# Kernel optimization log

Measured on AMD Instinct MI355X. Metric: run time of the kernel, lower is better.

## Reference

```python
import jax, jax.numpy as jnp
import numpy as np

E = 64  # hidden size (hardcoded in the module)
D = 50  # embedding dim (hardcoded)


def lstm_scan(xs, h0, c0, Wih, Whh, b):
    """xs: (S, B, in). PyTorch gate order i, f, g, o."""
    def step(carry, x):
        h, c = carry
        g = x @ Wih.T + h @ Whh.T + b
        i, f, gg, o = jnp.split(g, 4, axis=-1)
        c = jax.nn.sigmoid(f) * c + jax.nn.sigmoid(i) * jnp.tanh(gg)
        h = jax.nn.sigmoid(o) * jnp.tanh(c)
        return (h, c), (h, c)
    _, (hs, cs) = jax.lax.scan(step, (h0, c0), xs)
    return hs, cs  # (S, B, E)


def setup_inputs() -> dict:
    key = jax.random.key(0)
    ks = iter(jax.random.split(key, 40))
    B, S, V = 64, 384, 100004
    f32 = jnp.float32

    def rn(shape, scale):
        return (jax.random.normal(next(ks), shape, dtype=f32) * scale)

    km = float(np.sqrt(2.0 / E))       # kaiming_normal fan_in=64
    lu = float(1.0 / np.sqrt(E))       # torch LSTM default init scale

    inp = {
        "sentence1": jax.random.randint(next(ks), (B, S), 0, V),
        "sentence2": jax.random.randint(next(ks), (B, S), 0, V),
        "s1_len": jax.random.randint(next(ks), (B, 1, E), 0, S),
        "s2_len": jax.random.randint(next(ks), (B, 1, E), 0, S),
        "s1_s": jnp.ones((B, S), dtype=f32),
        "s2_s": jnp.ones((B, S), dtype=f32),
        "emb": rn((V, D), 0.1),
        "Wih1": rn((4 * E, D), lu), "Whh1": rn((4 * E, E), lu),
        "bih1": rn((4 * E,), lu), "bhh1": rn((4 * E,), lu),
        "Wih2": rn((4 * E, D), lu), "Whh2": rn((4 * E, E), lu),
        "bih2": rn((4 * E,), lu), "bhh2": rn((4 * E,), lu),
        "wy": rn((E, E), km), "wh": rn((E, E), km),
        "w": rn((E,), 1.0),
        "wp": rn((E, E), km), "wx": rn((E, E), km),
        "wr": rn((E, E), km), "wt": rn((E, E), km),
        "l1_W": rn((128, E), km), "l1_b": jnp.zeros((128,), f32),
        "l_W": rn((4, 128), float(np.sqrt(2.0 / 128))), "l_b": jnp.zeros((4,), f32),
    }
    return inp


def reference(sentence1, sentence2, s1_len, s2_len, s1_s, s2_s, emb,
              Wih1, Whh1, bih1, bhh1, Wih2, Whh2, bih2, bhh2,
              wy, wh, w, wp, wx, wr, wt, l1_W, l1_b, l_W, l_b):
    B, S = sentence1.shape
    e1 = emb[sentence1]  # (B,S,50)
    e2 = emb[sentence2]
    h0 = jnp.zeros((B, E), e1.dtype)

    # LSTMCell loop over sentence1, collecting all h/c
    hs, cs = lstm_scan(e1.transpose(1, 0, 2), h0, h0, Wih1, Whh1, bih1 + bhh1)
    h = hs.transpose(1, 0, 2)  # (B,S,E)
    c = cs.transpose(1, 0, 2)

    # gather initial state for lstm2 at s1_len indices
    gh = jnp.take_along_axis(h, s1_len, axis=1)[:, 0, :]
    gc = jnp.take_along_axis(c, s1_len, axis=1)[:, 0, :]

    os_, _ = lstm_scan(e2.transpose(1, 0, 2), gh, gc, Wih2, Whh2, bih2 + bhh2)
    out = os_.transpose(1, 0, 2)  # (B,S,E); note s2 == s per expand semantics

    # wyy + whhn are loop-invariant in the original (out.expand is identity)
    base = jnp.einsum('bse,ef->bsf', h, wy) + jnp.einsum('bse,ef->bsf', out, wh)
    NEG = jnp.float32(1e12)

    def att_step(r, _):
        M = jnp.tanh(base + (r @ wr)[:, None, :])          # (B,S,E)
        score = jnp.einsum('bse,e->bs', M, w)              # (B,S)
        masked = s1_s * score - (1.0 - s1_s) * NEG
        soft = jax.nn.softmax(masked, axis=1)
        r_new = jnp.einsum('bse,bs->be', h, soft) + jnp.tanh(r @ wt)
        return r_new, r_new

    r0 = jnp.zeros((B, E), h.dtype)
    _, Rt = jax.lax.scan(att_step, r0, None, length=S)
    Rt = Rt.transpose(1, 0, 2)  # (B,S,E)

    rn_ = jnp.take_along_axis(Rt, s2_len, axis=1)[:, 0, :]
    hn = jnp.take_along_axis(out, s2_len, axis=1)[:, 0, :]
    hid = jnp.tanh(rn_ @ wp + hn @ wx)
    hid = jnp.tanh(hid @ l1_W.T + l1_b)   # Dropout is inference-mode identity
    return hid @ l_W.T + l_b              # (B,4)
```

## Files before the change

### kernel.cpp

```cpp
#include <hip/hip_runtime.h>

#define E 64
#define D 50
#define SS 384
#define G4 256

__device__ __forceinline__ float fast_rcp(float x){ return __builtin_amdgcn_rcpf(x); }
__device__ __forceinline__ float tanh_fast(float x){
  float e = __expf(2.0f*x);
  return 1.0f - 2.0f*fast_rcp(e + 1.0f);
}
__device__ __forceinline__ float sigmoid_fast(float x){
  return fast_rcp(1.0f + __expf(-x));
}
__device__ __forceinline__ float rdlane(float v, int l){
  return __int_as_float(__builtin_amdgcn_readlane(__float_as_int(v), l));
}
#define DPP0(x, ctrl) __int_as_float(__builtin_amdgcn_update_dpp( \
    0, __float_as_int(x), ctrl, 0xF, 0xF, true))
__device__ __forceinline__ float wave_sum64_l63(float x){
  x += DPP0(x, 0x111);
  x += DPP0(x, 0x112);
  x += DPP0(x, 0x114);
  x += DPP0(x, 0x118);
  x += DPP0(x, 0x142);
  x += DPP0(x, 0x143);
  return x;
}
__device__ __forceinline__ void barrier_lds_only(){
  __builtin_amdgcn_sched_barrier(0);
  asm volatile("s_waitcnt lgkmcnt(0)" ::: "memory");
  __builtin_amdgcn_s_barrier();
  __builtin_amdgcn_sched_barrier(0);
}

__global__ __launch_bounds__(256, 1) void gx_kernel(
  const int* __restrict__ sent1, const int* __restrict__ sent2,
  const float* __restrict__ emb,
  const float* __restrict__ Wih1, const float* __restrict__ bih1, const float* __restrict__ bhh1,
  const float* __restrict__ Wih2, const float* __restrict__ bih2, const float* __restrict__ bhh2,
  float* __restrict__ gx1, float* __restrict__ gx2)
{
  const int bb    = blockIdx.x;
  const int which = bb >> 8;
  const int chunk = bb & 255;
  const int j     = threadIdx.x;
  const int*   sent = which ? sent2 : sent1;
  const float* Wih  = which ? Wih2  : Wih1;
  const float* bA   = which ? bih2  : bih1;
  const float* bB   = which ? bhh2  : bhh1;
  float*       gx   = which ? gx2   : gx1;

  float wih[D];
  #pragma unroll
  for (int k=0;k<D;k+=2){
    float2 v = *(const float2*)&Wih[j*D+k];
    wih[k]=v.x; wih[k+1]=v.y;
  }
  const float bias = bA[j] + bB[j];

  __shared__ __align__(16) float xb[8][52];
  const int row0 = chunk*96;
  for (int c=0;c<12;++c){
    const int r0 = row0 + c*8;
    #pragma unroll
    for (int q=0;q<2;++q){
      int tt = j + q*256;
      if (tt < 400){
        int r = tt/50;
        int k = tt - r*50;
        int idx = sent[r0 + r];
        xb[r][k] = emb[(size_t)idx*D + k];
      }
    }
    __syncthreads();
    for (int r=0;r<8;++r){
      float a0=bias, a1=0.f;
      #pragma unroll
      for (int k=0;k<48;k+=4){
        float4 xv = *(const float4*)&xb[r][k];
        a0 += xv.x*wih[k]   + xv.y*wih[k+1];
        a1 += xv.z*wih[k+2] + xv.w*wih[k+3];
      }
      a0 += xb[r][48]*wih[48];
      a1 += xb[r][49]*wih[49];
      gx[(size_t)(r0+r)*G4 + j] = a0+a1;
    }
    __syncthreads();
  }
}

__global__ __launch_bounds__(256, 1) void lstm_kernel(
  const float* __restrict__ gx1, const float* __restrict__ gx2,
  const float* __restrict__ Whh1, const float* __restrict__ Whh2,
  const int* __restrict__ s1_len, const int* __restrict__ s2_len,
  float* __restrict__ h1_all, float* __restrict__ out_all,
  float* __restrict__ hn_cap)
{
  const int b = blockIdx.x;
  const int j = threadIdx.x;
  const int lane = j & 63;
  const int wv = j >> 6;
  __shared__ float gates[2][256];
  __shared__ __align__(16) float hbuf[4][64];

  float whr[64];
  #pragma unroll
  for (int k=0;k<64;k+=4){
    float4 v = *(const float4*)&Whh1[j*64+k];
    whr[k]=v.x; whr[k+1]=v.y; whr[k+2]=v.z; whr[k+3]=v.w;
  }

  const int is_g = (wv==2);
  float c_reg=0.f, h_reg=0.f, gh=0.f, gc=0.f, hn=0.f;
  const int idx1 = s1_len[b*64+lane];
  const int idx2 = s2_len[b*64+lane];
  hbuf[wv][lane] = 0.f;

  {
    const float* gx = gx1 + (size_t)b*SS*G4;
    float* hout = h1_all + (size_t)b*SS*E;
    float gx_cur = gx[j];
    float gx_n1  = gx[G4 + j];
    float h_prev = 0.f;
    for (int s=0;s<SS;++s){
      int sn2 = (s+2<SS)? s+2 : SS-1;
      float gx_n2 = gx[(size_t)sn2*G4 + j];
      float g0=gx_cur, g1=0.f, g2=0.f, g3=0.f;
      #pragma unroll
      for (int k=0;k<64;k+=4){
        float4 hv = *(const float4*)&hbuf[wv][k];
        g0 = __builtin_fmaf(hv.x, whr[k],   g0);
        g1 = __builtin_fmaf(hv.y, whr[k+1], g1);
        g2 = __builtin_fmaf(hv.z, whr[k+2], g2);
        g3 = __builtin_fmaf(hv.w, whr[k+3], g3);
      }
      float g = (g0+g1)+(g2+g3);
      const int p = s & 1;
      gates[p][j] = is_g ? tanh_fast(g) : sigmoid_fast(g);
      barrier_lds_only();
      float gi=gates[p][lane], gf=gates[p][64+lane], gg=gates[p][128+lane], go=gates[p][192+lane];
      c_reg = gf*c_reg + gi*gg;
      h_reg = go * tanh_fast(c_reg);
      hbuf[wv][lane] = h_reg;
      if (wv==0 && s>0) hout[(size_t)(s-1)*E + lane] = h_prev;
      h_prev = h_reg;
      if (s==idx1){ gh=h_reg; gc=c_reg; }
      gx_cur = gx_n1; gx_n1 = gx_n2;
    }
    if (wv==0) hout[(size_t)(SS-1)*E + lane] = h_prev;
  }
  #pragma unroll
  for (int k=0;k<64;k+=4){
    float4 v = *(const float4*)&Whh2[j*64+k];
    whr[k]=v.x; whr[k+1]=v.y; whr[k+2]=v.z; whr[k+3]=v.w;
  }
  h_reg = gh; c_reg = gc;
  hbuf[wv][lane] = gh;
  barrier_lds_only();
  {
    const float* gx = gx2 + (size_t)b*SS*G4;
    float* hout = out_all + (size_t)b*SS*E;
    float gx_cur = gx[j];
    float gx_n1  = gx[G4 + j];
    float h_prev = 0.f;
    for (int s=0;s<SS;++s){
      int sn2 = (s+2<SS)? s+2 : SS-1;
      float gx_n2 = gx[(size_t)sn2*G4 + j];
      float g0=gx_cur, g1=0.f, g2=0.f, g3=0.f;
      #pragma unroll
      for (int k=0;k<64;k+=4){
        float4 hv = *(const float4*)&hbuf[wv][k];
        g0 = __builtin_fmaf(hv.x, whr[k],   g0);
        g1 = __builtin_fmaf(hv.y, whr[k+1], g1);
        g2 = __builtin_fmaf(hv.z, whr[k+2], g2);
        g3 = __builtin_fmaf(hv.w, whr[k+3], g3);
      }
      float g = (g0+g1)+(g2+g3);
      const int p = s & 1;
      gates[p][j] = is_g ? tanh_fast(g) : sigmoid_fast(g);
      barrier_lds_only();
      float gi=gates[p][lane], gf=gates[p][64+lane], gg=gates[p][128+lane], go=gates[p][192+lane];
      c_reg = gf*c_reg + gi*gg;
      h_reg = go * tanh_fast(c_reg);
      hbuf[wv][lane] = h_reg;
      if (wv==0 && s>0) hout[(size_t)(s-1)*E + lane] = h_prev;
      h_prev = h_reg;
      if (s==idx2) hn = h_reg;
      gx_cur = gx_n1; gx_n1 = gx_n2;
    }
    if (wv==0) hout[(size_t)(SS-1)*E + lane] = h_prev;
  }
  if (wv==0) hn_cap[b*64+lane] = hn;
}

__global__ __launch_bounds__(256, 1) void base_kernel(
  const float* __restrict__ h1_all, const float* __restrict__ out_all,
  const float* __restrict__ wy, const float* __restrict__ wh,
  float* __restrict__ E_g)
{
  const int t = threadIdx.x;
  const int wave = t>>6, lane = t&63;
  float wyc[E], whc[E];
  #pragma unroll
  for (int e=0;e<E;++e){ wyc[e]=wy[e*E+lane]; whc[e]=wh[e*E+lane]; }
  const int row0 = blockIdx.x*16 + wave*4;
  for (int r=0;r<4;++r){
    int row = row0 + r;
    float hv = h1_all[(size_t)row*E + lane];
    float ov = out_all[(size_t)row*E + lane];
    float a0=0,a1=0;
    #pragma unroll
    for (int e=0;e<E;++e){
      a0 += rdlane(hv,e)*wyc[e];
      a1 += rdlane(ov,e)*whc[e];
    }
    E_g[(size_t)row*E + lane] = __expf(2.0f*(a0+a1));
  }
}

__global__ __attribute__((amdgpu_flat_work_group_size(384,384), amdgpu_waves_per_eu(2,2)))
void attn_kernel(
  const float* __restrict__ h1_all, const float* __restrict__ E_all,
  const float* __restrict__ w, const float* __restrict__ wr, const float* __restrict__ wt,
  const float* __restrict__ s1_s, const int* __restrict__ s2_len,
  float* __restrict__ rn_cap)
{
  const int b = blockIdx.x;
  const int t = threadIdx.x;
  const int wv = t>>6, lane = t&63;
  const int row = wv*64 + lane;

  __shared__ float  accP[6*64];
  __shared__ float  totP[8];
  __shared__ float2 rwrtP[6*64];
  __shared__ __align__(16) float exL[6][64];
  __shared__ __align__(16) float RlL[6][64];

  const float* h1b = h1_all + (size_t)b*SS*E;
  const float* Eb  = E_all  + (size_t)b*SS*E;

  float Ee[64];
  #pragma unroll
  for (int k=0;k<64;k+=4){
    float4 v = *(const float4*)&Eb[(size_t)row*E + k];
    Ee[k]=v.x; Ee[k+1]=v.y; Ee[k+2]=v.z; Ee[k+3]=v.w;
  }
  float ht[64];
  #pragma unroll
  for (int i=0;i<64;++i){
    ht[i] = h1b[(size_t)(wv*64 + i)*E + lane];
  }
  float WSUM = 0.f;
  for (int e=0;e<64;++e) WSUM += w[e];
  const float s1v = s1_s[b*SS + row];
  const int  idx2 = s2_len[b*E + lane];
  const int k0  = (wv<4)? wv*11 : 44+(wv-4)*10;
  const int cnt = (wv<4)? 11 : 10;
  float wrch[11], wtch[11];
  #pragma unroll
  for (int jj=0;jj<11;++jj){
    int kk = k0 + ((jj<cnt)? jj : 0);
    wrch[jj] = wr[kk*E + lane];
    wtch[jj] = wt[kk*E + lane];
  }

  rwrtP[t] = make_float2(0.f, 0.f);
  __syncthreads();

  float rn_keep = 0.f;
  for (int s=0;s<SS;++s){
    float rwl=0.f, rtl=0.f;
    #pragma unroll
    for (int q=0;q<6;++q){ float2 v = rwrtP[q*64+lane]; rwl+=v.x; rtl+=v.y; }
    float Rl = __expf(2.0f*rwl);
    RlL[wv][lane] = Rl;

    float sc0=0.f, sc1=0.f, sc2=0.f, sc3=0.f;
    #pragma unroll
    for (int e=0;e<64;e+=8){
      float4 ra = *(const float4*)&RlL[wv][e];
      float4 rb = *(const float4*)&RlL[wv][e+4];
      float A  = __builtin_fmaf(Ee[e],  ra.x, 1.f);
      float B  = __builtin_fmaf(Ee[e+1],ra.y, 1.f);
      float C  = __builtin_fmaf(Ee[e+2],ra.z, 1.f);
      float Dv = __builtin_fmaf(Ee[e+3],ra.w, 1.f);
      float n0 = __builtin_fmaf(w[e],   B,  w[e+1]*A);
      float n1 = __builtin_fmaf(w[e+2], Dv, w[e+3]*C);
      sc0 = __builtin_fmaf(n0, fast_rcp(A*B),  sc0);
      sc1 = __builtin_fmaf(n1, fast_rcp(C*Dv), sc1);
      float A2  = __builtin_fmaf(Ee[e+4], rb.x, 1.f);
      float B2  = __builtin_fmaf(Ee[e+5], rb.y, 1.f);
      float C2  = __builtin_fmaf(Ee[e+6], rb.z, 1.f);
      float D2  = __builtin_fmaf(Ee[e+7], rb.w, 1.f);
      float n2 = __builtin_fmaf(w[e+4], B2, w[e+5]*A2);
      float n3 = __builtin_fmaf(w[e+6], D2, w[e+7]*C2);
      sc2 = __builtin_fmaf(n2, fast_rcp(A2*B2), sc2);
      sc3 = __builtin_fmaf(n3, fast_rcp(C2*D2), sc3);
    }
    float sc = WSUM - 2.0f*((sc0+sc1)+(sc2+sc3));
    float masked = s1v*sc - (1.f - s1v)*1e12f;
    float ex = __expf(masked);

    exL[wv][lane] = ex;
    float a0=0.f, a1=0.f, a2=0.f, a3=0.f;
    #pragma unroll
    for (int i=0;i<64;i+=4){
      float4 v = *(const float4*)&exL[wv][i];
      a0 = __builtin_fmaf(v.x, ht[i],   a0);
      a1 = __builtin_fmaf(v.y, ht[i+1], a1);
      a2 = __builtin_fmaf(v.z, ht[i+2], a2);
      a3 = __builtin_fmaf(v.w, ht[i+3], a3);
    }
    accP[wv*64+lane] = (a0+a1)+(a2+a3);
    float tw = wave_sum64_l63(ex);
    if (lane==63) totP[wv] = tw;
    __syncthreads();

    float av=0.f;
    #pragma unroll
    for (int q=0;q<6;++q) av += accP[q*64+lane];
    float tv = ((totP[0]+totP[1])+(totP[2]+totP[3]))+(totP[4]+totP[5]);
    float rnew = __builtin_fmaf(av, fast_rcp(tv), tanh_fast(rtl));
    if (wv==0 && s==idx2) rn_keep = rnew;
    float rwp=0.f, rtp=0.f;
    #pragma unroll
    for (int jj=0;jj<11;++jj){
      if (jj<cnt){
        float rv = rdlane(rnew, k0+jj);
        rwp = __builtin_fmaf(rv, wrch[jj], rwp);
        rtp = __builtin_fmaf(rv, wtch[jj], rtp);
      }
    }
    rwrtP[wv*64+lane] = make_float2(rwp, rtp);
    __syncthreads();
  }
  if (wv==0) rn_cap[b*E + lane] = rn_keep;
}

__global__ __launch_bounds__(128, 1) void final_kernel(
  const float* __restrict__ rn_cap, const float* __restrict__ hn_cap,
  const float* __restrict__ wp, const float* __restrict__ wx,
  const float* __restrict__ l1W, const float* __restrict__ l1b,
  const float* __restrict__ lW, const float* __restrict__ lb,
  float* __restrict__ out)
{
  const int b = blockIdx.x, t = threadIdx.x;
  __shared__ float rn[E], hn[E], hid1[E], hid2[128];
  if (t<E){ rn[t]=rn_cap[b*E+t]; hn[t]=hn_cap[b*E+t]; }
  __syncthreads();
  if (t<E){
    float a0=0,a1=0;
    #pragma unroll
    for (int k=0;k<E;++k){
      a0 += rn[k]*wp[k*E+t];
      a1 += hn[k]*wx[k*E+t];
    }
    hid1[t] = tanh_fast(a0+a1);
  }
  __syncthreads();
  {
    float acc = l1b[t];
    #pragma unroll
    for (int k=0;k<E;++k) acc += hid1[k]*l1W[t*E+k];
    hid2[t] = tanh_fast(acc);
  }
  __syncthreads();
  if (t<4){
    float acc = lb[t];
    #pragma unroll
    for (int k=0;k<128;++k) acc += hid2[k]*lW[t*128+k];
    out[b*4+t] = acc;
  }
}

extern "C" void kernel_launch(void* const* d_in, const int* in_sizes, int n_in,
                              void* d_out, int out_size, void* d_ws, size_t ws_size,
                              hipStream_t stream)
{
  const int*   sent1 = (const int*)  d_in[0];
  const int*   sent2 = (const int*)  d_in[1];
  const int*   s1len = (const int*)  d_in[2];
  const int*   s2len = (const int*)  d_in[3];
  const float* s1s   = (const float*)d_in[4];
  const float* emb   = (const float*)d_in[6];
  const float* Wih1  = (const float*)d_in[7];
  const float* Whh1  = (const float*)d_in[8];
  const float* bih1  = (const float*)d_in[9];
  const float* bhh1  = (const float*)d_in[10];
  const float* Wih2  = (const float*)d_in[11];
  const float* Whh2  = (const float*)d_in[12];
  const float* bih2  = (const float*)d_in[13];
  const float* bhh2  = (const float*)d_in[14];
  const float* wy    = (const float*)d_in[15];
  const float* wh    = (const float*)d_in[16];
  const float* w     = (const float*)d_in[17];
  const float* wp    = (const float*)d_in[18];
  const float* wx    = (const float*)d_in[19];
  const float* wr    = (const float*)d_in[20];
  const float* wt    = (const float*)d_in[21];
  const float* l1W   = (const float*)d_in[22];
  const float* l1b   = (const float*)d_in[23];
  const float* lW    = (const float*)d_in[24];
  const float* lb    = (const float*)d_in[25];
  float* out = (float*)d_out;

  float* ws  = (float*)d_ws;
  float* gx1 = ws;
  float* gx2 = gx1 + 6291456;
  float* h1  = gx2 + 6291456;
  float* outa= h1  + 1572864;
  float* Eg  = outa + 1572864;
  float* rnc = Eg  + 1572864;
  float* hnc = rnc + 4096;

  hipLaunchKernelGGL(gx_kernel, dim3(512), dim3(256), 0, stream,
    sent1, sent2, emb, Wih1, bih1, bhh1, Wih2, bih2, bhh2, gx1, gx2);
  hipLaunchKernelGGL(lstm_kernel, dim3(64), dim3(256), 0, stream,
    gx1, gx2, Whh1, Whh2, s1len, s2len, h1, outa, hnc);
  hipLaunchKernelGGL(base_kernel, dim3(1536), dim3(256), 0, stream,
    h1, outa, wy, wh, Eg);
  hipLaunchKernelGGL(attn_kernel, dim3(64), dim3(384), 0, stream,
    h1, Eg, w, wr, wt, s1s, s2len, rnc);
  hipLaunchKernelGGL(final_kernel, dim3(64), dim3(128), 0, stream,
    rnc, hnc, wp, wx, l1W, l1b, lW, lb, out);
}
```

Baseline: 1.329 ms.

## Pack two batch elements per workgroup in LSTM and attention kernels

```diff
diff --git a/kernel.cpp b/kernel.cpp
--- a/kernel.cpp
+++ b/kernel.cpp
@@ -90,46 +90,49 @@
   }
 }
 
-__global__ __launch_bounds__(256, 1) void lstm_kernel(
+__global__ __launch_bounds__(512, 1) void lstm_kernel(
   const float* __restrict__ gx1, const float* __restrict__ gx2,
   const float* __restrict__ Whh1, const float* __restrict__ Whh2,
   const int* __restrict__ s1_len, const int* __restrict__ s2_len,
   float* __restrict__ h1_all, float* __restrict__ out_all,
   float* __restrict__ hn_cap)
 {
-  const int b = blockIdx.x;
-  const int j = threadIdx.x;
-  const int lane = j & 63;
-  const int wv = j >> 6;
-  __shared__ float gates[2][256];
-  __shared__ __align__(16) float hbuf[4][64];
+  const int j    = threadIdx.x;
+  const int grp  = j >> 8;
+  const int jL   = j & 255;
+  const int b    = blockIdx.x*2 + grp;
+  const int lane = jL & 63;
+  const int wvL  = jL >> 6;
+  const int gw   = j >> 6;
+  __shared__ float gates[2][2][256];
+  __shared__ __align__(16) float hbuf[8][64];
 
   float whr[64];
   #pragma unroll
   for (int k=0;k<64;k+=4){
-    float4 v = *(const float4*)&Whh1[j*64+k];
+    float4 v = *(const float4*)&Whh1[jL*64+k];
     whr[k]=v.x; whr[k+1]=v.y; whr[k+2]=v.z; whr[k+3]=v.w;
   }
 
-  const int is_g = (wv==2);
+  const int is_g = (wvL==2);
   float c_reg=0.f, h_reg=0.f, gh=0.f, gc=0.f, hn=0.f;
   const int idx1 = s1_len[b*64+lane];
   const int idx2 = s2_len[b*64+lane];
-  hbuf[wv][lane] = 0.f;
+  hbuf[gw][lane] = 0.f;
 
   {
     const float* gx = gx1 + (size_t)b*SS*G4;
     float* hout = h1_all + (size_t)b*SS*E;
-    float gx_cur = gx[j];
-    float gx_n1  = gx[G4 + j];
+    float gx_cur = gx[jL];
+    float gx_n1  = gx[G4 + jL];
     float h_prev = 0.f;
     for (int s=0;s<SS;++s){
       int sn2 = (s+2<SS)? s+2 : SS-1;
-      float gx_n2 = gx[(size_t)sn2*G4 + j];
+      float gx_n2 = gx[(size_t)sn2*G4 + jL];
       float g0=gx_cur, g1=0.f, g2=0.f, g3=0.f;
       #pragma unroll
       for (int k=0;k<64;k+=4){
-        float4 hv = *(const float4*)&hbuf[wv][k];
+        float4 hv = *(const float4*)&hbuf[gw][k];
         g0 = __builtin_fmaf(hv.x, whr[k],   g0);
         g1 = __builtin_fmaf(hv.y, whr[k+1], g1);
         g2 = __builtin_fmaf(hv.z, whr[k+2], g2);
@@ -137,40 +140,41 @@
       }
       float g = (g0+g1)+(g2+g3);
       const int p = s & 1;
-      gates[p][j] = is_g ? tanh_fast(g) : sigmoid_fast(g);
+      gates[grp][p][jL] = is_g ? tanh_fast(g) : sigmoid_fast(g);
       barrier_lds_only();
-      float gi=gates[p][lane], gf=gates[p][64+lane], gg=gates[p][128+lane], go=gates[p][192+lane];
+      float gi=gates[grp][p][lane], gf=gates[grp][p][64+lane];
+      float gg=gates[grp][p][128+lane], go=gates[grp][p][192+lane];
       c_reg = gf*c_reg + gi*gg;
       h_reg = go * tanh_fast(c_reg);
-      hbuf[wv][lane] = h_reg;
-      if (wv==0 && s>0) hout[(size_t)(s-1)*E + lane] = h_prev;
+      hbuf[gw][lane] = h_reg;
+      if (wvL==0 && s>0) hout[(size_t)(s-1)*E + lane] = h_prev;
       h_prev = h_reg;
       if (s==idx1){ gh=h_reg; gc=c_reg; }
       gx_cur = gx_n1; gx_n1 = gx_n2;
     }
-    if (wv==0) hout[(size_t)(SS-1)*E + lane] = h_prev;
+    if (wvL==0) hout[(size_t)(SS-1)*E + lane] = h_prev;
   }
   #pragma unroll
   for (int k=0;k<64;k+=4){
-    float4 v = *(const float4*)&Whh2[j*64+k];
+    float4 v = *(const float4*)&Whh2[jL*64+k];
     whr[k]=v.x; whr[k+1]=v.y; whr[k+2]=v.z; whr[k+3]=v.w;
   }
   h_reg = gh; c_reg = gc;
-  hbuf[wv][lane] = gh;
+  hbuf[gw][lane] = gh;
   barrier_lds_only();
   {
     const float* gx = gx2 + (size_t)b*SS*G4;
     float* hout = out_all + (size_t)b*SS*E;
-    float gx_cur = gx[j];
-    float gx_n1  = gx[G4 + j];
+    float gx_cur = gx[jL];
+    float gx_n1  = gx[G4 + jL];
     float h_prev = 0.f;
     for (int s=0;s<SS;++s){
       int sn2 = (s+2<SS)? s+2 : SS-1;
-      float gx_n2 = gx[(size_t)sn2*G4 + j];
+      float gx_n2 = gx[(size_t)sn2*G4 + jL];
       float g0=gx_cur, g1=0.f, g2=0.f, g3=0.f;
       #pragma unroll
       for (int k=0;k<64;k+=4){
-        float4 hv = *(const float4*)&hbuf[wv][k];
+        float4 hv = *(const float4*)&hbuf[gw][k];
         g0 = __builtin_fmaf(hv.x, whr[k],   g0);
         g1 = __builtin_fmaf(hv.y, whr[k+1], g1);
         g2 = __builtin_fmaf(hv.z, whr[k+2], g2);
@@ -178,20 +182,21 @@
       }
       float g = (g0+g1)+(g2+g3);
       const int p = s & 1;
-      gates[p][j] = is_g ? tanh_fast(g) : sigmoid_fast(g);
+      gates[grp][p][jL] = is_g ? tanh_fast(g) : sigmoid_fast(g);
       barrier_lds_only();
-      float gi=gates[p][lane], gf=gates[p][64+lane], gg=gates[p][128+lane], go=gates[p][192+lane];
+      float gi=gates[grp][p][lane], gf=gates[grp][p][64+lane];
+      float gg=gates[grp][p][128+lane], go=gates[grp][p][192+lane];
       c_reg = gf*c_reg + gi*gg;
       h_reg = go * tanh_fast(c_reg);
-      hbuf[wv][lane] = h_reg;
-      if (wv==0 && s>0) hout[(size_t)(s-1)*E + lane] = h_prev;
+      hbuf[gw][lane] = h_reg;
+      if (wvL==0 && s>0) hout[(size_t)(s-1)*E + lane] = h_prev;
       h_prev = h_reg;
       if (s==idx2) hn = h_reg;
       gx_cur = gx_n1; gx_n1 = gx_n2;
     }
-    if (wv==0) hout[(size_t)(SS-1)*E + lane] = h_prev;
-  }
-  if (wv==0) hn_cap[b*64+lane] = hn;
+    if (wvL==0) hout[(size_t)(SS-1)*E + lane] = h_prev;
+  }
+  if (wvL==0) hn_cap[b*64+lane] = hn;
 }
 
 __global__ __launch_bounds__(256, 1) void base_kernel(
@@ -219,23 +224,25 @@
   }
 }
 
-__global__ __attribute__((amdgpu_flat_work_group_size(384,384), amdgpu_waves_per_eu(2,2)))
-void attn_kernel(
+__global__ __launch_bounds__(768, 1) void attn_kernel(
   const float* __restrict__ h1_all, const float* __restrict__ E_all,
   const float* __restrict__ w, const float* __restrict__ wr, const float* __restrict__ wt,
   const float* __restrict__ s1_s, const int* __restrict__ s2_len,
   float* __restrict__ rn_cap)
 {
-  const int b = blockIdx.x;
-  const int t = threadIdx.x;
-  const int wv = t>>6, lane = t&63;
+  const int t   = threadIdx.x;
+  const int grp = (t >= 384) ? 1 : 0;
+  const int tL  = t - 384*grp;
+  const int b   = blockIdx.x*2 + grp;
+  const int wv  = tL>>6, lane = tL&63;
+  const int gw  = grp*6 + wv;
   const int row = wv*64 + lane;
 
-  __shared__ float  accP[6*64];
-  __shared__ float  totP[8];
-  __shared__ float2 rwrtP[6*64];
-  __shared__ __align__(16) float exL[6][64];
-  __shared__ __align__(16) float RlL[6][64];
+  __shared__ float  accP[12*64];
+  __shared__ float  totP[2][8];
+  __shared__ float2 rwrtP[12*64];
+  __shared__ __align__(16) float exL[12][64];
+  __shared__ __align__(16) float RlL[12][64];
 
   const float* h1b = h1_all + (size_t)b*SS*E;
   const float* Eb  = E_all  + (size_t)b*SS*E;
@@ -265,22 +272,23 @@
     wtch[jj] = wt[kk*E + lane];
   }
 
-  rwrtP[t] = make_float2(0.f, 0.f);
+  rwrtP[gw*64+lane] = make_float2(0.f, 0.f);
   __syncthreads();
 
   float rn_keep = 0.f;
   for (int s=0;s<SS;++s){
     float rwl=0.f, rtl=0.f;
     #pragma unroll
-    for (int q=0;q<6;++q){ float2 v = rwrtP[q*64+lane]; rwl+=v.x; rtl+=v.y; }
+    for (int q=0;q<6;++q){ float2 v = rwrtP[(grp*6+q)*64+lane]; rwl+=v.x; rtl+=v.y; }
     float Rl = __expf(2.0f*rwl);
-    RlL[wv][lane] = Rl;
+    RlL[gw][lane] = Rl;
+    float trt = tanh_fast(rtl);
 
     float sc0=0.f, sc1=0.f, sc2=0.f, sc3=0.f;
     #pragma unroll
     for (int e=0;e<64;e+=8){
-      float4 ra = *(const float4*)&RlL[wv][e];
-      float4 rb = *(const float4*)&RlL[wv][e+4];
+      float4 ra = *(const float4*)&RlL[gw][e];
+      float4 rb = *(const float4*)&RlL[gw][e+4];
       float A  = __builtin_fmaf(Ee[e],  ra.x, 1.f);
       float B  = __builtin_fmaf(Ee[e+1],ra.y, 1.f);
       float C  = __builtin_fmaf(Ee[e+2],ra.z, 1.f);
@@ -302,26 +310,27 @@
     float masked = s1v*sc - (1.f - s1v)*1e12f;
     float ex = __expf(masked);
 
-    exL[wv][lane] = ex;
+    exL[gw][lane] = ex;
     float a0=0.f, a1=0.f, a2=0.f, a3=0.f;
     #pragma unroll
     for (int i=0;i<64;i+=4){
-      float4 v = *(const float4*)&exL[wv][i];
+      float4 v = *(const float4*)&exL[gw][i];
       a0 = __builtin_fmaf(v.x, ht[i],   a0);
       a1 = __builtin_fmaf(v.y, ht[i+1], a1);
       a2 = __builtin_fmaf(v.z, ht[i+2], a2);
       a3 = __builtin_fmaf(v.w, ht[i+3], a3);
     }
-    accP[wv*64+lane] = (a0+a1)+(a2+a3);
+    accP[gw*64+lane] = (a0+a1)+(a2+a3);
     float tw = wave_sum64_l63(ex);
-    if (lane==63) totP[wv] = tw;
+    if (lane==63) totP[grp][wv] = tw;
     __syncthreads();
 
     float av=0.f;
     #pragma unroll
-    for (int q=0;q<6;++q) av += accP[q*64+lane];
-    float tv = ((totP[0]+totP[1])+(totP[2]+totP[3]))+(totP[4]+totP[5]);
-    float rnew = __builtin_fmaf(av, fast_rcp(tv), tanh_fast(rtl));
+    for (int q=0;q<6;++q) av += accP[(grp*6+q)*64+lane];
+    float tv = ((totP[grp][0]+totP[grp][1])+(totP[grp][2]+totP[grp][3]))
+             + (totP[grp][4]+totP[grp][5]);
+    float rnew = __builtin_fmaf(av, fast_rcp(tv), trt);
     if (wv==0 && s==idx2) rn_keep = rnew;
     float rwp=0.f, rtp=0.f;
     #pragma unroll
@@ -332,7 +341,7 @@
         rtp = __builtin_fmaf(rv, wtch[jj], rtp);
       }
     }
-    rwrtP[wv*64+lane] = make_float2(rwp, rtp);
+    rwrtP[gw*64+lane] = make_float2(rwp, rtp);
     __syncthreads();
   }
   if (wv==0) rn_cap[b*E + lane] = rn_keep;
@@ -416,11 +425,11 @@
 
   hipLaunchKernelGGL(gx_kernel, dim3(512), dim3(256), 0, stream,
     sent1, sent2, emb, Wih1, bih1, bhh1, Wih2, bih2, bhh2, gx1, gx2);
-  hipLaunchKernelGGL(lstm_kernel, dim3(64), dim3(256), 0, stream,
+  hipLaunchKernelGGL(lstm_kernel, dim3(32), dim3(512), 0, stream,
     gx1, gx2, Whh1, Whh2, s1len, s2len, h1, outa, hnc);
   hipLaunchKernelGGL(base_kernel, dim3(1536), dim3(256), 0, stream,
     h1, outa, wy, wh, Eg);
-  hipLaunchKernelGGL(attn_kernel, dim3(64), dim3(384), 0, stream,
+  hipLaunchKernelGGL(attn_kernel, dim3(32), dim3(768), 0, stream,
     h1, Eg, w, wr, wt, s1s, s2len, rnc);
   hipLaunchKernelGGL(final_kernel, dim3(64), dim3(128), 0, stream,
     rnc, hnc, wp, wx, l1W, l1b, lW, lb, out);
```

Result: slower. 2.827 ms (+112.8%).

## Spread attention rows over 8 waves of 48 rows each

Applied to the files above, without the earlier changes.

```diff
diff --git a/kernel.cpp b/kernel.cpp
--- a/kernel.cpp
+++ b/kernel.cpp
@@ -219,7 +219,8 @@
   }
 }
 
-__global__ __attribute__((amdgpu_flat_work_group_size(384,384), amdgpu_waves_per_eu(2,2)))
+#define RPW 48
+__global__ __attribute__((amdgpu_flat_work_group_size(512,512), amdgpu_waves_per_eu(2,2)))
 void attn_kernel(
   const float* __restrict__ h1_all, const float* __restrict__ E_all,
   const float* __restrict__ w, const float* __restrict__ wr, const float* __restrict__ wt,
@@ -229,13 +230,14 @@
   const int b = blockIdx.x;
   const int t = threadIdx.x;
   const int wv = t>>6, lane = t&63;
-  const int row = wv*64 + lane;
-
-  __shared__ float  accP[6*64];
+  const bool owner = (lane < RPW);
+  const int row = wv*RPW + (owner ? lane : RPW-1);
+
+  __shared__ float  accP[8*64];
   __shared__ float  totP[8];
-  __shared__ float2 rwrtP[6*64];
-  __shared__ __align__(16) float exL[6][64];
-  __shared__ __align__(16) float RlL[6][64];
+  __shared__ float2 rwrtP[8*64];
+  __shared__ __align__(16) float exL[8][RPW];
+  __shared__ __align__(16) float RlL[8][64];
 
   const float* h1b = h1_all + (size_t)b*SS*E;
   const float* Eb  = E_all  + (size_t)b*SS*E;
@@ -246,35 +248,34 @@
     float4 v = *(const float4*)&Eb[(size_t)row*E + k];
     Ee[k]=v.x; Ee[k+1]=v.y; Ee[k+2]=v.z; Ee[k+3]=v.w;
   }
-  float ht[64];
-  #pragma unroll
-  for (int i=0;i<64;++i){
-    ht[i] = h1b[(size_t)(wv*64 + i)*E + lane];
+  float ht[RPW];
+  #pragma unroll
+  for (int i=0;i<RPW;++i){
+    ht[i] = h1b[(size_t)(wv*RPW + i)*E + lane];
   }
   float WSUM = 0.f;
   for (int e=0;e<64;++e) WSUM += w[e];
   const float s1v = s1_s[b*SS + row];
   const int  idx2 = s2_len[b*E + lane];
-  const int k0  = (wv<4)? wv*11 : 44+(wv-4)*10;
-  const int cnt = (wv<4)? 11 : 10;
-  float wrch[11], wtch[11];
-  #pragma unroll
-  for (int jj=0;jj<11;++jj){
-    int kk = k0 + ((jj<cnt)? jj : 0);
-    wrch[jj] = wr[kk*E + lane];
-    wtch[jj] = wt[kk*E + lane];
-  }
-
-  rwrtP[t] = make_float2(0.f, 0.f);
+  const int k0 = wv*8;
+  float wrch[8], wtch[8];
+  #pragma unroll
+  for (int jj=0;jj<8;++jj){
+    wrch[jj] = wr[(k0+jj)*E + lane];
+    wtch[jj] = wt[(k0+jj)*E + lane];
+  }
+
+  rwrtP[t&511] = make_float2(0.f, 0.f);
   __syncthreads();
 
   float rn_keep = 0.f;
   for (int s=0;s<SS;++s){
     float rwl=0.f, rtl=0.f;
     #pragma unroll
-    for (int q=0;q<6;++q){ float2 v = rwrtP[q*64+lane]; rwl+=v.x; rtl+=v.y; }
+    for (int q=0;q<8;++q){ float2 v = rwrtP[q*64+lane]; rwl+=v.x; rtl+=v.y; }
     float Rl = __expf(2.0f*rwl);
     RlL[wv][lane] = Rl;
+    float trt = tanh_fast(rtl);
 
     float sc0=0.f, sc1=0.f, sc2=0.f, sc3=0.f;
     #pragma unroll
@@ -302,10 +303,10 @@
     float masked = s1v*sc - (1.f - s1v)*1e12f;
     float ex = __expf(masked);
 
-    exL[wv][lane] = ex;
+    if (owner) exL[wv][lane] = ex;
     float a0=0.f, a1=0.f, a2=0.f, a3=0.f;
     #pragma unroll
-    for (int i=0;i<64;i+=4){
+    for (int i=0;i<RPW;i+=4){
       float4 v = *(const float4*)&exL[wv][i];
       a0 = __builtin_fmaf(v.x, ht[i],   a0);
       a1 = __builtin_fmaf(v.y, ht[i+1], a1);
@@ -313,24 +314,24 @@
       a3 = __builtin_fmaf(v.w, ht[i+3], a3);
     }
     accP[wv*64+lane] = (a0+a1)+(a2+a3);
-    float tw = wave_sum64_l63(ex);
+    float exm = owner ? ex : 0.f;
+    float tw = wave_sum64_l63(exm);
     if (lane==63) totP[wv] = tw;
     __syncthreads();
 
     float av=0.f;
     #pragma unroll
-    for (int q=0;q<6;++q) av += accP[q*64+lane];
-    float tv = ((totP[0]+totP[1])+(totP[2]+totP[3]))+(totP[4]+totP[5]);
-    float rnew = __builtin_fmaf(av, fast_rcp(tv), tanh_fast(rtl));
+    for (int q=0;q<8;++q) av += accP[q*64+lane];
+    float tv = ((totP[0]+totP[1])+(totP[2]+totP[3]))
+             + ((totP[4]+totP[5])+(totP[6]+totP[7]));
+    float rnew = __builtin_fmaf(av, fast_rcp(tv), trt);
     if (wv==0 && s==idx2) rn_keep = rnew;
     float rwp=0.f, rtp=0.f;
     #pragma unroll
-    for (int jj=0;jj<11;++jj){
-      if (jj<cnt){
-        float rv = rdlane(rnew, k0+jj);
-        rwp = __builtin_fmaf(rv, wrch[jj], rwp);
-        rtp = __builtin_fmaf(rv, wtch[jj], rtp);
-      }
+    for (int jj=0;jj<8;++jj){
+      float rv = rdlane(rnew, k0+jj);
+      rwp = __builtin_fmaf(rv, wrch[jj], rwp);
+      rtp = __builtin_fmaf(rv, wtch[jj], rtp);
     }
     rwrtP[wv*64+lane] = make_float2(rwp, rtp);
     __syncthreads();
@@ -420,7 +421,7 @@
     gx1, gx2, Whh1, Whh2, s1len, s2len, h1, outa, hnc);
   hipLaunchKernelGGL(base_kernel, dim3(1536), dim3(256), 0, stream,
     h1, outa, wy, wh, Eg);
-  hipLaunchKernelGGL(attn_kernel, dim3(64), dim3(384), 0, stream,
+  hipLaunchKernelGGL(attn_kernel, dim3(64), dim3(512), 0, stream,
     h1, Eg, w, wr, wt, s1s, s2len, rnc);
   hipLaunchKernelGGL(final_kernel, dim3(64), dim3(128), 0, stream,
     rnc, hnc, wp, wx, l1W, l1b, lW, lb, out);
```

New measurement: 1.746 ms. +31.4%, slower.
